# Kernel tuning notes

Hardware: AMD Instinct MI355X
Metric: run time of the kernel (lower is better)

Reference implementation:

```python
import jax, jax.numpy as jnp
import numpy as np

N_NODES = 100000
N_EDGES = 1600000
IN_FEATS = 128
OUT_FEATS = 48


def setup_inputs() -> dict:
    key = jax.random.key(0)
    ks = jax.random.split(key, 6)
    features = jax.random.normal(ks[0], (N_NODES, IN_FEATS), dtype=jnp.float32)
    # xavier_uniform for W.weight [out, in]
    lim_w = float(np.sqrt(6.0 / (IN_FEATS + OUT_FEATS)))
    W_w = jax.random.uniform(ks[1], (OUT_FEATS, IN_FEATS), dtype=jnp.float32, minval=-lim_w, maxval=lim_w)
    W_b = jnp.zeros((OUT_FEATS,), dtype=jnp.float32)
    # xavier_uniform for attn_w [2*out, 1]
    lim_a = float(np.sqrt(6.0 / (2 * OUT_FEATS + 1)))
    attn_w = jax.random.uniform(ks[2], (2 * OUT_FEATS, 1), dtype=jnp.float32, minval=-lim_a, maxval=lim_a)
    attn_b = jnp.zeros((1,), dtype=jnp.float32)
    src = jax.random.randint(ks[3], (N_EDGES,), 0, N_NODES, dtype=jnp.int32)
    dst = jax.random.randint(ks[4], (N_EDGES,), 0, N_NODES, dtype=jnp.int32)
    return {"features": features, "W_w": W_w, "W_b": W_b,
            "attn_w": attn_w, "attn_b": attn_b, "src": src, "dst": dst}


def reference(features, W_w, W_b, attn_w, attn_b, src, dst):
    n = features.shape[0]
    d = W_w.shape[0]
    # h = W(features)  [N, d]
    h = features @ W_w.T + W_b
    # cat([h[src], h[dst]]) @ attn_w == h[src] @ w_src + h[dst] @ w_dst
    w_src = attn_w[:d, 0]   # [d]
    w_dst = attn_w[d:, 0]   # [d]
    s_src = h @ w_src       # [N]
    s_dst = h @ w_dst       # [N]
    e = s_src[src] + s_dst[dst] + attn_b[0]            # [E]
    e = jax.nn.leaky_relu(e, negative_slope=0.2)
    # edge softmax grouped by destination node
    m = jax.ops.segment_max(e, dst, num_segments=n)     # [N]
    ex = jnp.exp(e - m[dst])                            # [E]
    denom = jax.ops.segment_sum(ex, dst, num_segments=n)  # [N]
    alpha = ex / denom[dst]                             # [E]
    # weighted scatter-sum: out[v] = sum_{(u,v) in E} alpha * h[u]
    msgs = h[src] * alpha[:, None]                      # [E, d]
    out = jax.ops.segment_sum(msgs, dst, num_segments=n)  # [N, d]
    return out
```

## Files before the change

kernel.cpp:

```cpp
#include <hip/hip_runtime.h>

#define NFEAT 128
#define DOUT 48
#define BSH 6
#define BNODES 64
#define PCAP 192
#define BCAP (PCAP * 8)
#define EPT 16
#define NBMAX 1568

__device__ __forceinline__ float bf_lo(unsigned u) { return __uint_as_float(u << 16); }
__device__ __forceinline__ float bf_hi(unsigned u) { return __uint_as_float(u & 0xFFFF0000u); }
__device__ __forceinline__ unsigned bf_pack(float a, float b) {
    unsigned ua = __float_as_uint(a), ub = __float_as_uint(b);
    ua = (ua + 0x7FFFu + ((ua >> 16) & 1u)) >> 16;
    ub = (ub + 0x7FFFu + ((ub >> 16) & 1u)) & 0xFFFF0000u;
    return ua | ub;
}

__global__ __launch_bounds__(256) void k_proj(
    const float* __restrict__ feat, const float* __restrict__ Ww,
    const float* __restrict__ Wb, const float* __restrict__ attn_w,
    unsigned* __restrict__ hbf, float* __restrict__ s_src, float* __restrict__ s_dst,
    int n)
{
    __shared__ float hbA[64][49];
    __shared__ float hbB[64][49];

    int tid  = threadIdx.x;
    int lane = tid & 63;
    int kq   = __builtin_amdgcn_readfirstlane(tid >> 6);
    int gnode = blockIdx.x * 64 + lane;
    bool live = (gnode < n);

    float hv[DOUT];
#pragma unroll
    for (int j = 0; j < DOUT; ++j) hv[j] = 0.f;

    if (live) {
        const float4* fp = (const float4*)(feat + (size_t)gnode * NFEAT + kq * 32);
        float4 f[8];
#pragma unroll
        for (int i = 0; i < 8; ++i) f[i] = fp[i];
#pragma unroll
        for (int j = 0; j < DOUT; ++j) {
            const float4* wp = (const float4*)(Ww + (size_t)j * NFEAT + kq * 32);
            float acc = hv[j];
#pragma unroll
            for (int i = 0; i < 8; ++i) {
                float4 w = wp[i];
                acc = fmaf(f[i].x, w.x, acc);
                acc = fmaf(f[i].y, w.y, acc);
                acc = fmaf(f[i].z, w.z, acc);
                acc = fmaf(f[i].w, w.w, acc);
            }
            hv[j] = acc;
        }
    }

    float (*hb)[49] = (kq < 2) ? hbA : hbB;
    if ((kq & 1) == 0) {
#pragma unroll
        for (int j = 0; j < DOUT; ++j) hb[lane][j] = hv[j];
    }
    __syncthreads();
    if ((kq & 1) == 1) {
#pragma unroll
        for (int j = 0; j < DOUT; ++j) hb[lane][j] += hv[j];
    }
    __syncthreads();

    int node = tid >> 2, part = tid & 3, jb = part * 12;
    int gn2 = blockIdx.x * 64 + node;
    float v[12];
#pragma unroll
    for (int j = 0; j < 12; ++j) v[j] = hbA[node][jb + j] + hbB[node][jb + j] + Wb[jb + j];

    float ss = 0.f, sd = 0.f;
#pragma unroll
    for (int j = 0; j < 12; ++j) {
        ss = fmaf(v[j], attn_w[jb + j], ss);
        sd = fmaf(v[j], attn_w[DOUT + jb + j], sd);
    }
    ss += __shfl_xor(ss, 1, 64); ss += __shfl_xor(ss, 2, 64);
    sd += __shfl_xor(sd, 1, 64); sd += __shfl_xor(sd, 2, 64);

    if (gn2 < n) {
        uint2* hp = (uint2*)(hbf + (size_t)gn2 * 24 + part * 6);
#pragma unroll
        for (int q = 0; q < 3; ++q) {
            uint2 u;
            u.x = bf_pack(v[4 * q + 0], v[4 * q + 1]);
            u.y = bf_pack(v[4 * q + 2], v[4 * q + 3]);
            hp[q] = u;
        }
        if (part == 0) {
            s_src[gn2] = ss;
            s_dst[gn2] = sd;
        }
    }
}

__global__ __launch_bounds__(256) void k_bin(
    const int4* __restrict__ src4, const int4* __restrict__ dst4,
    const float* __restrict__ s_src, const float* __restrict__ s_dst,
    const float* __restrict__ attn_b,
    int* __restrict__ cursor, int2* __restrict__ ents, int nE, int NB)
{
    __shared__ int hist[NBMAX];
    __shared__ int bas[NBMAX];

    int tid = threadIdx.x;
    int cls = blockIdx.x & 7;
    long long e0 = (long long)blockIdx.x * 4096 + (long long)tid * EPT;

    for (int t = tid; t < NB; t += 256) hist[t] = 0;
    __syncthreads();

    int s[EPT], d[EPT];
    bool any = (e0 < nE);
#pragma unroll
    for (int q = 0; q < EPT / 4; ++q) {
        int4 sv = any ? src4[e0 / 4 + q] : make_int4(0, 0, 0, 0);
        int4 dv = any ? dst4[e0 / 4 + q] : make_int4(0, 0, 0, 0);
        s[4 * q + 0] = sv.x; s[4 * q + 1] = sv.y; s[4 * q + 2] = sv.z; s[4 * q + 3] = sv.w;
        d[4 * q + 0] = dv.x; d[4 * q + 1] = dv.y; d[4 * q + 2] = dv.z; d[4 * q + 3] = dv.w;
    }

    float vs[EPT], vd[EPT];
#pragma unroll
    for (int u = 0; u < EPT; ++u) vs[u] = s_src[s[u]];
#pragma unroll
    for (int u = 0; u < EPT; ++u) vd[u] = s_dst[d[u]];

    int rank[EPT];
#pragma unroll
    for (int u = 0; u < EPT; ++u)
        rank[u] = (e0 + u < nE) ? atomicAdd(&hist[d[u] >> BSH], 1) : 0;
    __syncthreads();

    for (int t = tid; t < NB; t += 256) {
        int c = hist[t];
        if (c > 0) bas[t] = atomicAdd(cursor + cls * NB + t, c);
    }
    __syncthreads();

    float ab = attn_b[0];
#pragma unroll
    for (int u = 0; u < EPT; ++u) {
        if (e0 + u < nE) {
            float v = vs[u] + vd[u] + ab;
            v = (v > 0.f) ? v : 0.2f * v;
            float x = __expf(v);
            int bkt = d[u] >> BSH;
            int slot = bas[bkt] + rank[u];
            if (slot < PCAP)
                ents[(size_t)bkt * BCAP + cls * PCAP + slot] =
                    make_int2(s[u] | ((d[u] & (BNODES - 1)) << 17), __float_as_int(x));
        }
    }
}

__global__ __launch_bounds__(256) void k_aggb(
    const unsigned* __restrict__ hbf, const int* __restrict__ cursor,
    const int2* __restrict__ ents, float* __restrict__ out, int n, int NB)
{
    __shared__ int2 se[BCAP];
    __shared__ unsigned short sidx[BCAP];
    __shared__ int c1[BNODES], c2[BNODES], lrp[BNODES + 1];
    __shared__ int cp[9];

    int b = blockIdx.x;
    int tid = threadIdx.x;

    if (tid < BNODES) { c1[tid] = 0; c2[tid] = 0; }
    __syncthreads();
    if (tid == 0) {
        int r = 0;
        for (int c = 0; c < 8; ++c) {
            cp[c] = r;
            r += min(cursor[c * NB + b], PCAP);
        }
        cp[8] = r;
    }
    __syncthreads();
    int total = cp[8];

    for (int i = tid; i < total; i += 256) {
        int c = 0;
        while (i >= cp[c + 1]) ++c;
        int2 v = ents[(size_t)b * BCAP + c * PCAP + (i - cp[c])];
        se[i] = v;
        atomicAdd(&c1[((unsigned)v.x) >> 17], 1);
    }
    __syncthreads();

    if (tid < BNODES) {
        int v = c1[tid];
        int p = v;
#pragma unroll
        for (int o = 1; o < 64; o <<= 1) {
            int u = __shfl_up(p, o, 64);
            if (tid >= o) p += u;
        }
        lrp[tid] = p - v;
        if (tid == BNODES - 1) lrp[BNODES] = p;
    }
    __syncthreads();

    for (int i = tid; i < total; i += 256) {
        int dl = ((unsigned)se[i].x) >> 17;
        int pos = lrp[dl] + atomicAdd(&c2[dl], 1);
        sidx[pos] = (unsigned short)i;
    }
    __syncthreads();

    int wave = tid >> 6, lane = tid & 63;
    int g = lane >> 3, sub = lane & 7;
    for (int dl = wave; dl < BNODES; dl += 4) {
        int node = (b << BSH) + dl;
        if (node >= n) break;
        int st = lrp[dl], en = lrp[dl + 1];
        float a0 = 0.f, a1 = 0.f, a2 = 0.f, a3 = 0.f, a4 = 0.f, a5 = 0.f, den = 0.f;
        for (int k = st + g; k < en; k += 8) {
            int2 ed = se[sidx[k]];
            float x = __int_as_float(ed.y);
            den += x;
            const unsigned* hr = hbf + (size_t)(ed.x & 0x1FFFF) * 24 + sub * 3;
            unsigned u0 = hr[0], u1 = hr[1], u2 = hr[2];
            a0 = fmaf(x, bf_lo(u0), a0);
            a1 = fmaf(x, bf_hi(u0), a1);
            a2 = fmaf(x, bf_lo(u1), a2);
            a3 = fmaf(x, bf_hi(u1), a3);
            a4 = fmaf(x, bf_lo(u2), a4);
            a5 = fmaf(x, bf_hi(u2), a5);
        }
#pragma unroll
        for (int o = 8; o <= 32; o <<= 1) {
            a0  += __shfl_xor(a0, o, 64);
            a1  += __shfl_xor(a1, o, 64);
            a2  += __shfl_xor(a2, o, 64);
            a3  += __shfl_xor(a3, o, 64);
            a4  += __shfl_xor(a4, o, 64);
            a5  += __shfl_xor(a5, o, 64);
            den += __shfl_xor(den, o, 64);
        }
        if (lane < 8) {
            float inv = (en > st) ? 1.f / den : 0.f;
            float* op = out + (size_t)node * DOUT + sub * 6;
            op[0] = a0 * inv;
            op[1] = a1 * inv;
            op[2] = a2 * inv;
            op[3] = a3 * inv;
            op[4] = a4 * inv;
            op[5] = a5 * inv;
        }
    }
}

extern "C" void kernel_launch(void* const* d_in, const int* in_sizes, int n_in,
                              void* d_out, int out_size, void* d_ws, size_t ws_size,
                              hipStream_t stream) {
    const float* feat   = (const float*)d_in[0];
    const float* Ww     = (const float*)d_in[1];
    const float* Wb     = (const float*)d_in[2];
    const float* attn_w = (const float*)d_in[3];
    const float* attn_b = (const float*)d_in[4];
    const int*   src    = (const int*)d_in[5];
    const int*   dst    = (const int*)d_in[6];

    int n  = in_sizes[0] / NFEAT;
    int nE = in_sizes[5];
    int NB = (n + BNODES - 1) / BNODES;
    int N8 = NB * 8;
    float* out = (float*)d_out;

    unsigned* hbf  = (unsigned*)d_ws;
    float* s_src   = (float*)(hbf + (size_t)n * 24);
    float* s_dst   = s_src + n;
    int*   cursor  = (int*)(s_dst + n);
    int2*  ents    = (int2*)(cursor + N8);

    hipMemsetAsync(cursor, 0, (size_t)N8 * sizeof(int), stream);

    k_proj<<<NB, 256, 0, stream>>>(feat, Ww, Wb, attn_w, hbf, s_src, s_dst, n);
    int nbb = (nE + 4095) / 4096;
    k_bin<<<nbb, 256, 0, stream>>>((const int4*)src, (const int4*)dst,
                                   s_src, s_dst, attn_b, cursor, ents, nE, NB);
    k_aggb<<<NB, 256, 0, stream>>>(hbf, cursor, ents, out, n, NB);
}
```

Before: 203.0 us.

## Compute node projection with split-bf16 MFMA instead of scalar FMAs

The projection kernel is rewritten to use 16x16x32 bf16 MFMA instructions. Each fp32 operand is split into hi and lo bf16 parts and three MFMAs per tile recover near-fp32 accuracy. Each block now covers 128 nodes instead of 64, the k-split LDS reduction becomes a single LDS staging buffer, and the bf16 stores are widened. This targets the scalar FMA cost of the feature projection. It adds split-conversion ALU work and a small loss of precision from dropping the lo*lo term.

New measurement: 193.3 us. 4.8% less time.

```diff
diff --git a/kernel.cpp b/kernel.cpp
--- a/kernel.cpp
+++ b/kernel.cpp
@@ -9,6 +9,9 @@
 #define EPT 16
 #define NBMAX 1568
 
+typedef __attribute__((ext_vector_type(8))) short bf16x8;
+typedef __attribute__((ext_vector_type(4))) float f32x4;
+
 __device__ __forceinline__ float bf_lo(unsigned u) { return __uint_as_float(u << 16); }
 __device__ __forceinline__ float bf_hi(unsigned u) { return __uint_as_float(u & 0xFFFF0000u); }
 __device__ __forceinline__ unsigned bf_pack(float a, float b) {
@@ -18,85 +21,124 @@
     return ua | ub;
 }
 
+__device__ __forceinline__ void split2(float x, short& hi, short& lo) {
+    unsigned u = __float_as_uint(x);
+    unsigned h = u & 0xFFFF0000u;
+    hi = (short)(h >> 16);
+    float r = x - __uint_as_float(h);
+    unsigned v = __float_as_uint(r);
+    lo = (short)((v + 0x7FFFu + ((v >> 16) & 1u)) >> 16);
+}
+
 __global__ __launch_bounds__(256) void k_proj(
     const float* __restrict__ feat, const float* __restrict__ Ww,
     const float* __restrict__ Wb, const float* __restrict__ attn_w,
     unsigned* __restrict__ hbf, float* __restrict__ s_src, float* __restrict__ s_dst,
     int n)
 {
-    __shared__ float hbA[64][49];
-    __shared__ float hbB[64][49];
+    __shared__ float hb[128][49];
 
     int tid  = threadIdx.x;
     int lane = tid & 63;
-    int kq   = __builtin_amdgcn_readfirstlane(tid >> 6);
-    int gnode = blockIdx.x * 64 + lane;
-    bool live = (gnode < n);
-
-    float hv[DOUT];
-#pragma unroll
-    for (int j = 0; j < DOUT; ++j) hv[j] = 0.f;
-
-    if (live) {
-        const float4* fp = (const float4*)(feat + (size_t)gnode * NFEAT + kq * 32);
-        float4 f[8];
-#pragma unroll
-        for (int i = 0; i < 8; ++i) f[i] = fp[i];
-#pragma unroll
-        for (int j = 0; j < DOUT; ++j) {
-            const float4* wp = (const float4*)(Ww + (size_t)j * NFEAT + kq * 32);
-            float acc = hv[j];
-#pragma unroll
-            for (int i = 0; i < 8; ++i) {
-                float4 w = wp[i];
-                acc = fmaf(f[i].x, w.x, acc);
-                acc = fmaf(f[i].y, w.y, acc);
-                acc = fmaf(f[i].z, w.z, acc);
-                acc = fmaf(f[i].w, w.w, acc);
+    int wv   = tid >> 6;
+    int g    = lane >> 4;
+    int r16  = lane & 15;
+
+    int mbase = blockIdx.x * 128 + wv * 32;
+    int na0 = mbase + r16;       if (na0 >= n) na0 = n - 1;
+    int na1 = mbase + 16 + r16;  if (na1 >= n) na1 = n - 1;
+
+    const float* fA0 = feat + (size_t)na0 * NFEAT + g * 4;
+    const float* fA1 = feat + (size_t)na1 * NFEAT + g * 4;
+    const float* wB  = Ww + (size_t)r16 * NFEAT + g * 4;
+
+    f32x4 acc[2][3];
+#pragma unroll
+    for (int mt = 0; mt < 2; ++mt)
+#pragma unroll
+        for (int nt = 0; nt < 3; ++nt)
+            acc[mt][nt] = (f32x4){0.f, 0.f, 0.f, 0.f};
+
+#pragma unroll
+    for (int ks = 0; ks < 4; ++ks) {
+        f32x4 ra[4], rb[6];
+        ra[0] = *(const f32x4*)(fA0 + ks * 32);
+        ra[1] = *(const f32x4*)(fA0 + ks * 32 + 16);
+        ra[2] = *(const f32x4*)(fA1 + ks * 32);
+        ra[3] = *(const f32x4*)(fA1 + ks * 32 + 16);
+        rb[0] = *(const f32x4*)(wB + ks * 32);
+        rb[1] = *(const f32x4*)(wB + ks * 32 + 16);
+        rb[2] = *(const f32x4*)(wB + 16 * NFEAT + ks * 32);
+        rb[3] = *(const f32x4*)(wB + 16 * NFEAT + ks * 32 + 16);
+        rb[4] = *(const f32x4*)(wB + 32 * NFEAT + ks * 32);
+        rb[5] = *(const f32x4*)(wB + 32 * NFEAT + ks * 32 + 16);
+
+        bf16x8 Ah[2], Al[2], Bh[3], Bl[3];
+#pragma unroll
+        for (int t = 0; t < 2; ++t) {
+#pragma unroll
+            for (int i = 0; i < 4; ++i) {
+                short h, l;
+                split2(ra[2 * t][i], h, l);     Ah[t][i] = h;     Al[t][i] = l;
+                split2(ra[2 * t + 1][i], h, l); Ah[t][i + 4] = h; Al[t][i + 4] = l;
             }
-            hv[j] = acc;
-        }
-    }
-
-    float (*hb)[49] = (kq < 2) ? hbA : hbB;
-    if ((kq & 1) == 0) {
-#pragma unroll
-        for (int j = 0; j < DOUT; ++j) hb[lane][j] = hv[j];
-    }
-    __syncthreads();
-    if ((kq & 1) == 1) {
-#pragma unroll
-        for (int j = 0; j < DOUT; ++j) hb[lane][j] += hv[j];
-    }
-    __syncthreads();
-
-    int node = tid >> 2, part = tid & 3, jb = part * 12;
-    int gn2 = blockIdx.x * 64 + node;
-    float v[12];
-#pragma unroll
-    for (int j = 0; j < 12; ++j) v[j] = hbA[node][jb + j] + hbB[node][jb + j] + Wb[jb + j];
-
+        }
+#pragma unroll
+        for (int t = 0; t < 3; ++t) {
+#pragma unroll
+            for (int i = 0; i < 4; ++i) {
+                short h, l;
+                split2(rb[2 * t][i], h, l);     Bh[t][i] = h;     Bl[t][i] = l;
+                split2(rb[2 * t + 1][i], h, l); Bh[t][i + 4] = h; Bl[t][i + 4] = l;
+            }
+        }
+#pragma unroll
+        for (int mt = 0; mt < 2; ++mt)
+#pragma unroll
+            for (int nt = 0; nt < 3; ++nt) {
+                acc[mt][nt] = __builtin_amdgcn_mfma_f32_16x16x32_bf16(Ah[mt], Bh[nt], acc[mt][nt], 0, 0, 0);
+                acc[mt][nt] = __builtin_amdgcn_mfma_f32_16x16x32_bf16(Al[mt], Bh[nt], acc[mt][nt], 0, 0, 0);
+                acc[mt][nt] = __builtin_amdgcn_mfma_f32_16x16x32_bf16(Ah[mt], Bl[nt], acc[mt][nt], 0, 0, 0);
+            }
+    }
+
+#pragma unroll
+    for (int mt = 0; mt < 2; ++mt)
+#pragma unroll
+        for (int nt = 0; nt < 3; ++nt)
+#pragma unroll
+            for (int rr = 0; rr < 4; ++rr)
+                hb[wv * 32 + mt * 16 + 4 * g + rr][nt * 16 + r16] = acc[mt][nt][rr];
+    __syncthreads();
+
+    int node = tid >> 1, part = tid & 1, jb = part * 24;
+    int gn = blockIdx.x * 128 + node;
+    float v[24];
     float ss = 0.f, sd = 0.f;
 #pragma unroll
-    for (int j = 0; j < 12; ++j) {
-        ss = fmaf(v[j], attn_w[jb + j], ss);
-        sd = fmaf(v[j], attn_w[DOUT + jb + j], sd);
-    }
-    ss += __shfl_xor(ss, 1, 64); ss += __shfl_xor(ss, 2, 64);
-    sd += __shfl_xor(sd, 1, 64); sd += __shfl_xor(sd, 2, 64);
-
-    if (gn2 < n) {
-        uint2* hp = (uint2*)(hbf + (size_t)gn2 * 24 + part * 6);
+    for (int j = 0; j < 24; ++j) {
+        float x = hb[node][jb + j] + Wb[jb + j];
+        v[j] = x;
+        ss = fmaf(x, attn_w[jb + j], ss);
+        sd = fmaf(x, attn_w[DOUT + jb + j], sd);
+    }
+    ss += __shfl_xor(ss, 1, 64);
+    sd += __shfl_xor(sd, 1, 64);
+
+    if (gn < n) {
+        uint4* hp = (uint4*)(hbf + (size_t)gn * 24 + part * 12);
 #pragma unroll
         for (int q = 0; q < 3; ++q) {
-            uint2 u;
-            u.x = bf_pack(v[4 * q + 0], v[4 * q + 1]);
-            u.y = bf_pack(v[4 * q + 2], v[4 * q + 3]);
+            uint4 u;
+            u.x = bf_pack(v[8 * q + 0], v[8 * q + 1]);
+            u.y = bf_pack(v[8 * q + 2], v[8 * q + 3]);
+            u.z = bf_pack(v[8 * q + 4], v[8 * q + 5]);
+            u.w = bf_pack(v[8 * q + 6], v[8 * q + 7]);
             hp[q] = u;
         }
         if (part == 0) {
-            s_src[gn2] = ss;
-            s_dst[gn2] = sd;
+            s_src[gn] = ss;
+            s_dst[gn] = sd;
         }
     }
 }
@@ -283,7 +325,8 @@
 
     hipMemsetAsync(cursor, 0, (size_t)N8 * sizeof(int), stream);
 
-    k_proj<<<NB, 256, 0, stream>>>(feat, Ww, Wb, attn_w, hbf, s_src, s_dst, n);
+    int NBp = (n + 127) / 128;
+    k_proj<<<NBp, 256, 0, stream>>>(feat, Ww, Wb, attn_w, hbf, s_src, s_dst, n);
     int nbb = (nE + 4095) / 4096;
     k_bin<<<nbb, 256, 0, stream>>>((const int4*)src, (const int4*)dst,
                                    s_src, s_dst, attn_b, cursor, ents, nE, NB);
```
